# Performance work log

Hardware: AMD Instinct MI355X
Metric: run time of the kernel (lower is better)

The kernel has to match this reference:

```python
import jax, jax.numpy as jnp
import numpy as np

B, T, N, D = 16, 48, 256, 64
K_HEADS = 8


def setup_inputs() -> dict:
    key = jax.random.key(0)
    ks = jax.random.split(key, 12)
    return {
        "query": jax.random.normal(ks[0], (B, T, N, D), jnp.float32),
        "key": jax.random.normal(ks[1], (B, T, N, D), jnp.float32),
        "value": jax.random.normal(ks[2], (B, T, N, D), jnp.float32),
        "key_w": jax.random.normal(ks[3], (B, T, D, D), jnp.float32) * 0.05,
        "key_b": jax.random.normal(ks[4], (B, T, D), jnp.float32) * 0.05,
        "value_w": jax.random.normal(ks[5], (B, T, D, D), jnp.float32) * 0.05,
        "value_b": jax.random.normal(ks[6], (B, T, D), jnp.float32) * 0.05,
        "proj1_w": jax.random.normal(ks[7], (D, D), jnp.float32) * 0.05,
        "proj1_b": jax.random.normal(ks[8], (D,), jnp.float32) * 0.05,
        "proj2_w": jax.random.normal(ks[9], (D, D), jnp.float32) * 0.05,
        "proj2_b": jax.random.normal(ks[10], (D,), jnp.float32) * 0.05,
        "rate": jnp.full((1,), 0.8, jnp.float32),
    }


def reference(query, key, value, key_w, key_b, value_w, value_b,
              proj1_w, proj1_b, proj2_w, proj2_b, rate):
    b, t, n, d = query.shape
    hs = d // K_HEADS
    # per-(batch,time) projections (LinearCustom)
    k = jnp.einsum('btnd,btde->btne', key, key_w) + key_b[:, :, None, :]
    v = jnp.einsum('btnd,btde->btne', value, value_w) + value_b[:, :, None, :]
    # split heads along channel dim (matches torch.split on dim -1)
    qh = query.reshape(b, t, n, K_HEADS, hs)
    kh = k.reshape(b, t, n, K_HEADS, hs)
    vh = v.reshape(b, t, n, K_HEADS, hs)
    # scores: [b, h, n, q, k]
    scores = jnp.einsum('bqnhd,bknhd->bhnqk', qh, kh) / jnp.sqrt(jnp.asarray(hs, query.dtype))
    # time decay: b_time_decays[..., i, j] = (T-1-i) + 1 = T - i (depends on query pos only)
    dec = (t - jnp.arange(t, dtype=scores.dtype))[:, None]  # [T, 1], broadcasts over key axis
    s = jax.nn.sigmoid(scores)
    denom = 1.0 + jax.nn.sigmoid(s * jax.nn.sigmoid(rate) * dec)
    att = jax.nn.softmax(jnp.tanh(s / denom), axis=-1)
    x = jnp.einsum('bhnqk,bknhd->bqnhd', att, vh).reshape(b, t, n, d)
    x = jnp.tanh(x @ proj1_w.T + proj1_b)
    return x @ proj2_w.T + proj2_b
```

## Files before the change

kernel.cpp:

```cpp
#include <hip/hip_runtime.h>


#define B_ 16
#define T_ 48
#define N_ 256
#define D_ 64
#define H_ 8
#define HS_ 8

__device__ __forceinline__ float rcpf(float x) { return __builtin_amdgcn_rcpf(x); }

__global__ __launch_bounds__(256) void proj_kv_kernel(
    const float* __restrict__ key, const float* __restrict__ key_w, const float* __restrict__ key_b,
    const float* __restrict__ value, const float* __restrict__ value_w, const float* __restrict__ value_b,
    float* __restrict__ k_out, float* __restrict__ v_out)
{
    const int bt = blockIdx.x;
    const int which = blockIdx.y;
    const float* __restrict__ in = (which ? value : key) + (size_t)bt * N_ * D_;
    const float* __restrict__ w  = (which ? value_w : key_w) + (size_t)bt * D_ * D_;
    const float* __restrict__ bb = (which ? value_b : key_b) + (size_t)bt * D_;
    float* __restrict__ out = (which ? v_out : k_out) + (size_t)bt * N_ * D_;

    __shared__ float Wl[D_][D_];
    __shared__ float Xl[64][D_ + 1];
    __shared__ float Bl[D_];

    const int tid = threadIdx.x;
    #pragma unroll
    for (int i = tid; i < D_ * D_; i += 256) Wl[i >> 6][i & 63] = w[i];
    if (tid < D_) Bl[tid] = bb[tid];

    const int tc = tid & 15;
    const int tr = tid >> 4;

    for (int n0 = 0; n0 < N_; n0 += 64) {
        __syncthreads();
        #pragma unroll
        for (int i = tid; i < 64 * D_; i += 256) Xl[i >> 6][i & 63] = in[(size_t)n0 * D_ + i];
        __syncthreads();

        float acc[4][4];
        #pragma unroll
        for (int j = 0; j < 4; ++j) {
            #pragma unroll
            for (int i = 0; i < 4; ++i) acc[j][i] = Bl[tc * 4 + i];
        }

        #pragma unroll 8
        for (int d = 0; d < D_; ++d) {
            const float4 bv = *(const float4*)&Wl[d][tc * 4];
            #pragma unroll
            for (int j = 0; j < 4; ++j) {
                const float a = Xl[tr * 4 + j][d];
                acc[j][0] += a * bv.x;
                acc[j][1] += a * bv.y;
                acc[j][2] += a * bv.z;
                acc[j][3] += a * bv.w;
            }
        }

        #pragma unroll
        for (int j = 0; j < 4; ++j) {
            const float4 st = make_float4(acc[j][0], acc[j][1], acc[j][2], acc[j][3]);
            *(float4*)&out[(size_t)(n0 + tr * 4 + j) * D_ + tc * 4] = st;
        }
    }
}

__global__ __launch_bounds__(384) void attn_kernel(
    const float* __restrict__ query, float* __restrict__ k_xatt, const float* __restrict__ v_in,
    const float* __restrict__ rate)
{
    const int b = blockIdx.x >> 8;
    const int n = blockIdx.x & 255;

    __shared__ float Q[T_][68];
    __shared__ float K[T_][68];
    __shared__ float V[T_][68];

    const int tid = threadIdx.x;
    #pragma unroll
    for (int i = tid; i < T_ * D_; i += 384) {
        const int t = i >> 6, d = i & 63;
        const size_t g = ((size_t)(b * T_ + t) * N_ + n) * D_ + d;
        Q[t][d] = query[g];
        K[t][d] = k_xatt[g];
        V[t][d] = v_in[g];
    }
    const float rsig = rcpf(1.0f + __expf(-rate[0]));
    __syncthreads();

    const int q = tid % 48;
    const int h = tid / 48;
    float qf[8];
    #pragma unroll
    for (int d = 0; d < 8; ++d) qf[d] = Q[q][h * 8 + d];
    const float rd = rsig * (float)(T_ - q);

    float acc[8] = {0.f, 0.f, 0.f, 0.f, 0.f, 0.f, 0.f, 0.f};
    float ssum = 0.f;
    #pragma unroll 4
    for (int tk = 0; tk < T_; ++tk) {
        float sc = 0.f;
        #pragma unroll
        for (int d = 0; d < 8; ++d) sc += qf[d] * K[tk][h * 8 + d];
        sc *= 0.35355339059327373f;
        const float s   = rcpf(1.0f + __expf(-sc));
        const float s2  = rcpf(1.0f + __expf(-s * rd));
        const float arg = s * rcpf(1.0f + s2);
        const float th  = 1.0f - 2.0f * rcpf(__expf(2.0f * arg) + 1.0f);
        const float e   = __expf(th);
        ssum += e;
        #pragma unroll
        for (int d = 0; d < 8; ++d) acc[d] += e * V[tk][h * 8 + d];
    }
    const float inv = rcpf(ssum);

    __syncthreads();
    #pragma unroll
    for (int d = 0; d < 8; ++d) Q[q][h * 8 + d] = acc[d] * inv;
    __syncthreads();

    #pragma unroll
    for (int i = tid; i < T_ * D_; i += 384) {
        const int t = i >> 6, d = i & 63;
        k_xatt[((size_t)(b * T_ + t) * N_ + n) * D_ + d] = Q[t][d];
    }
}

__global__ __launch_bounds__(512) void out_proj_kernel(
    const float* __restrict__ xatt,
    const float* __restrict__ p1w, const float* __restrict__ p1b,
    const float* __restrict__ p2w, const float* __restrict__ p2b,
    float* __restrict__ out)
{
    __shared__ float W1t[D_][68];
    __shared__ float W2t[D_][68];
    __shared__ float X[64][68];
    __shared__ float B1[D_], B2[D_];

    const int tid = threadIdx.x;
    const size_t m0 = (size_t)blockIdx.x * 64;

    #pragma unroll
    for (int i = tid; i < D_ * D_; i += 512) {
        const int c = i >> 6, d = i & 63;
        W1t[d][c] = p1w[i];
        W2t[d][c] = p2w[i];
    }
    #pragma unroll
    for (int i = tid; i < 64 * D_; i += 512) X[i >> 6][i & 63] = xatt[m0 * D_ + i];
    if (tid < D_) { B1[tid] = p1b[tid]; B2[tid] = p2b[tid]; }
    __syncthreads();

    const int cg = tid & 7;
    const int r  = tid >> 3;

    float x1[8];
    {
        float a[8];
        #pragma unroll
        for (int i = 0; i < 8; ++i) a[i] = B1[cg * 8 + i];
        #pragma unroll 8
        for (int d = 0; d < D_; ++d) {
            const float xv = X[r][d];
            const float4 w0 = *(const float4*)&W1t[d][cg * 8];
            const float4 w1 = *(const float4*)&W1t[d][cg * 8 + 4];
            a[0] += xv * w0.x; a[1] += xv * w0.y; a[2] += xv * w0.z; a[3] += xv * w0.w;
            a[4] += xv * w1.x; a[5] += xv * w1.y; a[6] += xv * w1.z; a[7] += xv * w1.w;
        }
        #pragma unroll
        for (int i = 0; i < 8; ++i)
            x1[i] = 1.0f - 2.0f * rcpf(__expf(2.0f * a[i]) + 1.0f);
    }
    __syncthreads();
    #pragma unroll
    for (int i = 0; i < 8; ++i) X[r][cg * 8 + i] = x1[i];
    __syncthreads();

    {
        float a[8];
        #pragma unroll
        for (int i = 0; i < 8; ++i) a[i] = B2[cg * 8 + i];
        #pragma unroll 8
        for (int d = 0; d < D_; ++d) {
            const float xv = X[r][d];
            const float4 w0 = *(const float4*)&W2t[d][cg * 8];
            const float4 w1 = *(const float4*)&W2t[d][cg * 8 + 4];
            a[0] += xv * w0.x; a[1] += xv * w0.y; a[2] += xv * w0.z; a[3] += xv * w0.w;
            a[4] += xv * w1.x; a[5] += xv * w1.y; a[6] += xv * w1.z; a[7] += xv * w1.w;
        }
        const size_t og = (m0 + r) * D_ + cg * 8;
        *(float4*)&out[og]     = make_float4(a[0], a[1], a[2], a[3]);
        *(float4*)&out[og + 4] = make_float4(a[4], a[5], a[6], a[7]);
    }
}

extern "C" void kernel_launch(void* const* d_in, const int* in_sizes, int n_in,
                              void* d_out, int out_size, void* d_ws, size_t ws_size,
                              hipStream_t stream) {
    const float* query   = (const float*)d_in[0];
    const float* key     = (const float*)d_in[1];
    const float* value   = (const float*)d_in[2];
    const float* key_w   = (const float*)d_in[3];
    const float* key_b   = (const float*)d_in[4];
    const float* value_w = (const float*)d_in[5];
    const float* value_b = (const float*)d_in[6];
    const float* p1w     = (const float*)d_in[7];
    const float* p1b     = (const float*)d_in[8];
    const float* p2w     = (const float*)d_in[9];
    const float* p2b     = (const float*)d_in[10];
    const float* rate    = (const float*)d_in[11];
    float* out = (float*)d_out;

    float* kws = (float*)d_ws;
    float* vws = kws + (size_t)B_ * T_ * N_ * D_;

    dim3 gridA(B_ * T_, 2);
    proj_kv_kernel<<<gridA, 256, 0, stream>>>(key, key_w, key_b, value, value_w, value_b, kws, vws);
    attn_kernel<<<B_ * N_, 384, 0, stream>>>(query, kws, vws, rate);
    out_proj_kernel<<<(B_ * T_ * N_) / 64, 512, 0, stream>>>(kws, p1w, p1b, p2w, p2b, out);
}
```

Measured before the change: 259.3 us.

## Widen register tiles, vectorize loads, and use exp2 in all three kernels

Changes the K/V projection kernel to process 128 rows per pass with an 8-column-per-thread register tile. The out-projection kernel now handles 128 rows per block with two rows per thread, so weight loads from shared memory are reused more. Global and shared loads and stores become float4 in all kernels. The attention math is rewritten with exp2 and constants folded into the query scale. Larger per-thread tiles raise register pressure and halve the out-projection grid, which may lower occupancy.

```diff
diff --git a/kernel.cpp b/kernel.cpp
--- a/kernel.cpp
+++ b/kernel.cpp
@@ -9,6 +9,9 @@
 #define HS_ 8
 
 __device__ __forceinline__ float rcpf(float x) { return __builtin_amdgcn_rcpf(x); }
+__device__ __forceinline__ float ex2(float x) { return __builtin_amdgcn_exp2f(x); }
+
+#define LOG2E 1.4426950408889634f
 
 __global__ __launch_bounds__(256) void proj_kv_kernel(
     const float* __restrict__ key, const float* __restrict__ key_w, const float* __restrict__ key_b,
@@ -23,7 +26,7 @@
     float* __restrict__ out = (which ? v_out : k_out) + (size_t)bt * N_ * D_;
 
     __shared__ float Wl[D_][D_];
-    __shared__ float Xl[64][D_ + 1];
+    __shared__ float Xl[128][68];
     __shared__ float Bl[D_];
 
     const int tid = threadIdx.x;
@@ -31,39 +34,43 @@
     for (int i = tid; i < D_ * D_; i += 256) Wl[i >> 6][i & 63] = w[i];
     if (tid < D_) Bl[tid] = bb[tid];
 
-    const int tc = tid & 15;
-    const int tr = tid >> 4;
-
-    for (int n0 = 0; n0 < N_; n0 += 64) {
+    const int cg = tid & 7;
+    const int rg = tid >> 3;
+
+    for (int n0 = 0; n0 < N_; n0 += 128) {
         __syncthreads();
         #pragma unroll
-        for (int i = tid; i < 64 * D_; i += 256) Xl[i >> 6][i & 63] = in[(size_t)n0 * D_ + i];
+        for (int i = tid; i < 128 * D_ / 4; i += 256) {
+            const int e = i * 4;
+            *(float4*)&Xl[e >> 6][e & 63] = *(const float4*)&in[(size_t)n0 * D_ + e];
+        }
         __syncthreads();
 
-        float acc[4][4];
-        #pragma unroll
-        for (int j = 0; j < 4; ++j) {
+        float acc[4][8];
+        #pragma unroll
+        for (int j = 0; j < 4; ++j)
             #pragma unroll
-            for (int i = 0; i < 4; ++i) acc[j][i] = Bl[tc * 4 + i];
-        }
+            for (int i = 0; i < 8; ++i) acc[j][i] = Bl[cg * 8 + i];
 
         #pragma unroll 8
         for (int d = 0; d < D_; ++d) {
-            const float4 bv = *(const float4*)&Wl[d][tc * 4];
+            const float4 w0 = *(const float4*)&Wl[d][cg * 8];
+            const float4 w1 = *(const float4*)&Wl[d][cg * 8 + 4];
             #pragma unroll
             for (int j = 0; j < 4; ++j) {
-                const float a = Xl[tr * 4 + j][d];
-                acc[j][0] += a * bv.x;
-                acc[j][1] += a * bv.y;
-                acc[j][2] += a * bv.z;
-                acc[j][3] += a * bv.w;
+                const float a = Xl[rg + 32 * j][d];
+                acc[j][0] += a * w0.x; acc[j][1] += a * w0.y;
+                acc[j][2] += a * w0.z; acc[j][3] += a * w0.w;
+                acc[j][4] += a * w1.x; acc[j][5] += a * w1.y;
+                acc[j][6] += a * w1.z; acc[j][7] += a * w1.w;
             }
         }
 
         #pragma unroll
         for (int j = 0; j < 4; ++j) {
-            const float4 st = make_float4(acc[j][0], acc[j][1], acc[j][2], acc[j][3]);
-            *(float4*)&out[(size_t)(n0 + tr * 4 + j) * D_ + tc * 4] = st;
+            const size_t row = (size_t)(n0 + rg + 32 * j);
+            *(float4*)&out[row * D_ + cg * 8]     = make_float4(acc[j][0], acc[j][1], acc[j][2], acc[j][3]);
+            *(float4*)&out[row * D_ + cg * 8 + 4] = make_float4(acc[j][4], acc[j][5], acc[j][6], acc[j][7]);
         }
     }
 }
@@ -81,51 +88,61 @@
 
     const int tid = threadIdx.x;
     #pragma unroll
-    for (int i = tid; i < T_ * D_; i += 384) {
-        const int t = i >> 6, d = i & 63;
+    for (int i = tid; i < T_ * D_ / 4; i += 384) {
+        const int e = i * 4;
+        const int t = e >> 6, d = e & 63;
         const size_t g = ((size_t)(b * T_ + t) * N_ + n) * D_ + d;
-        Q[t][d] = query[g];
-        K[t][d] = k_xatt[g];
-        V[t][d] = v_in[g];
-    }
-    const float rsig = rcpf(1.0f + __expf(-rate[0]));
+        *(float4*)&Q[t][d] = *(const float4*)&query[g];
+        *(float4*)&K[t][d] = *(const float4*)&k_xatt[g];
+        *(float4*)&V[t][d] = *(const float4*)&v_in[g];
+    }
+    const float rsig = rcpf(1.0f + ex2(-rate[0] * LOG2E));
     __syncthreads();
 
     const int q = tid % 48;
     const int h = tid / 48;
-    float qf[8];
-    #pragma unroll
-    for (int d = 0; d < 8; ++d) qf[d] = Q[q][h * 8 + d];
-    const float rd = rsig * (float)(T_ - q);
-
-    float acc[8] = {0.f, 0.f, 0.f, 0.f, 0.f, 0.f, 0.f, 0.f};
+
+    const float C1 = 0.35355339059327373f * LOG2E;
+    float4 qa = *(const float4*)&Q[q][h * 8];
+    float4 qb = *(const float4*)&Q[q][h * 8 + 4];
+    qa.x *= -C1; qa.y *= -C1; qa.z *= -C1; qa.w *= -C1;
+    qb.x *= -C1; qb.y *= -C1; qb.z *= -C1; qb.w *= -C1;
+    const float rdn = -rsig * (float)(T_ - q) * LOG2E;
+
+    float4 acc0 = make_float4(0.f, 0.f, 0.f, 0.f);
+    float4 acc1 = make_float4(0.f, 0.f, 0.f, 0.f);
     float ssum = 0.f;
     #pragma unroll 4
     for (int tk = 0; tk < T_; ++tk) {
-        float sc = 0.f;
-        #pragma unroll
-        for (int d = 0; d < 8; ++d) sc += qf[d] * K[tk][h * 8 + d];
-        sc *= 0.35355339059327373f;
-        const float s   = rcpf(1.0f + __expf(-sc));
-        const float s2  = rcpf(1.0f + __expf(-s * rd));
+        const float4 ka = *(const float4*)&K[tk][h * 8];
+        const float4 kb = *(const float4*)&K[tk][h * 8 + 4];
+        const float dn = qa.x * ka.x + qa.y * ka.y + qa.z * ka.z + qa.w * ka.w
+                       + qb.x * kb.x + qb.y * kb.y + qb.z * kb.z + qb.w * kb.w;
+        const float s   = rcpf(1.0f + ex2(dn));
+        const float s2  = rcpf(1.0f + ex2(s * rdn));
         const float arg = s * rcpf(1.0f + s2);
-        const float th  = 1.0f - 2.0f * rcpf(__expf(2.0f * arg) + 1.0f);
-        const float e   = __expf(th);
+        const float th  = 1.0f - 2.0f * rcpf(ex2(arg * (2.0f * LOG2E)) + 1.0f);
+        const float e   = ex2(th * LOG2E);
         ssum += e;
-        #pragma unroll
-        for (int d = 0; d < 8; ++d) acc[d] += e * V[tk][h * 8 + d];
+        const float4 va = *(const float4*)&V[tk][h * 8];
+        const float4 vb = *(const float4*)&V[tk][h * 8 + 4];
+        acc0.x += e * va.x; acc0.y += e * va.y; acc0.z += e * va.z; acc0.w += e * va.w;
+        acc1.x += e * vb.x; acc1.y += e * vb.y; acc1.z += e * vb.z; acc1.w += e * vb.w;
     }
     const float inv = rcpf(ssum);
 
     __syncthreads();
-    #pragma unroll
-    for (int d = 0; d < 8; ++d) Q[q][h * 8 + d] = acc[d] * inv;
-    __syncthreads();
-
-    #pragma unroll
-    for (int i = tid; i < T_ * D_; i += 384) {
-        const int t = i >> 6, d = i & 63;
-        k_xatt[((size_t)(b * T_ + t) * N_ + n) * D_ + d] = Q[t][d];
+    acc0.x *= inv; acc0.y *= inv; acc0.z *= inv; acc0.w *= inv;
+    acc1.x *= inv; acc1.y *= inv; acc1.z *= inv; acc1.w *= inv;
+    *(float4*)&Q[q][h * 8]     = acc0;
+    *(float4*)&Q[q][h * 8 + 4] = acc1;
+    __syncthreads();
+
+    #pragma unroll
+    for (int i = tid; i < T_ * D_ / 4; i += 384) {
+        const int e = i * 4;
+        const int t = e >> 6, d = e & 63;
+        *(float4*)&k_xatt[((size_t)(b * T_ + t) * N_ + n) * D_ + d] = *(const float4*)&Q[t][d];
     }
 }
 
@@ -137,11 +154,11 @@
 {
     __shared__ float W1t[D_][68];
     __shared__ float W2t[D_][68];
-    __shared__ float X[64][68];
+    __shared__ float X[128][68];
     __shared__ float B1[D_], B2[D_];
 
     const int tid = threadIdx.x;
-    const size_t m0 = (size_t)blockIdx.x * 64;
+    const size_t m0 = (size_t)blockIdx.x * 128;
 
     #pragma unroll
     for (int i = tid; i < D_ * D_; i += 512) {
@@ -150,50 +167,67 @@
         W2t[d][c] = p2w[i];
     }
     #pragma unroll
-    for (int i = tid; i < 64 * D_; i += 512) X[i >> 6][i & 63] = xatt[m0 * D_ + i];
+    for (int i = tid; i < 128 * D_ / 4; i += 512) {
+        const int e = i * 4;
+        *(float4*)&X[e >> 6][e & 63] = *(const float4*)&xatt[m0 * D_ + e];
+    }
     if (tid < D_) { B1[tid] = p1b[tid]; B2[tid] = p2b[tid]; }
     __syncthreads();
 
     const int cg = tid & 7;
-    const int r  = tid >> 3;
-
-    float x1[8];
+    const int rp = tid >> 3;
+
+    float x1a[8], x1b[8];
     {
-        float a[8];
-        #pragma unroll
-        for (int i = 0; i < 8; ++i) a[i] = B1[cg * 8 + i];
+        float a[8], b2r[8];
+        #pragma unroll
+        for (int i = 0; i < 8; ++i) { a[i] = B1[cg * 8 + i]; b2r[i] = B1[cg * 8 + i]; }
         #pragma unroll 8
         for (int d = 0; d < D_; ++d) {
-            const float xv = X[r][d];
+            const float xv0 = X[rp][d];
+            const float xv1 = X[rp + 64][d];
             const float4 w0 = *(const float4*)&W1t[d][cg * 8];
             const float4 w1 = *(const float4*)&W1t[d][cg * 8 + 4];
-            a[0] += xv * w0.x; a[1] += xv * w0.y; a[2] += xv * w0.z; a[3] += xv * w0.w;
-            a[4] += xv * w1.x; a[5] += xv * w1.y; a[6] += xv * w1.z; a[7] += xv * w1.w;
-        }
-        #pragma unroll
-        for (int i = 0; i < 8; ++i)
-            x1[i] = 1.0f - 2.0f * rcpf(__expf(2.0f * a[i]) + 1.0f);
-    }
-    __syncthreads();
-    #pragma unroll
-    for (int i = 0; i < 8; ++i) X[r][cg * 8 + i] = x1[i];
+            a[0] += xv0 * w0.x; a[1] += xv0 * w0.y; a[2] += xv0 * w0.z; a[3] += xv0 * w0.w;
+            a[4] += xv0 * w1.x; a[5] += xv0 * w1.y; a[6] += xv0 * w1.z; a[7] += xv0 * w1.w;
+            b2r[0] += xv1 * w0.x; b2r[1] += xv1 * w0.y; b2r[2] += xv1 * w0.z; b2r[3] += xv1 * w0.w;
+            b2r[4] += xv1 * w1.x; b2r[5] += xv1 * w1.y; b2r[6] += xv1 * w1.z; b2r[7] += xv1 * w1.w;
+        }
+        #pragma unroll
+        for (int i = 0; i < 8; ++i) {
+            x1a[i] = 1.0f - 2.0f * rcpf(ex2(a[i]   * (2.0f * LOG2E)) + 1.0f);
+            x1b[i] = 1.0f - 2.0f * rcpf(ex2(b2r[i] * (2.0f * LOG2E)) + 1.0f);
+        }
+    }
+    __syncthreads();
+    #pragma unroll
+    for (int i = 0; i < 8; ++i) {
+        X[rp][cg * 8 + i]      = x1a[i];
+        X[rp + 64][cg * 8 + i] = x1b[i];
+    }
     __syncthreads();
 
     {
-        float a[8];
-        #pragma unroll
-        for (int i = 0; i < 8; ++i) a[i] = B2[cg * 8 + i];
+        float a[8], b2r[8];
+        #pragma unroll
+        for (int i = 0; i < 8; ++i) { a[i] = B2[cg * 8 + i]; b2r[i] = B2[cg * 8 + i]; }
         #pragma unroll 8
         for (int d = 0; d < D_; ++d) {
-            const float xv = X[r][d];
+            const float xv0 = X[rp][d];
+            const float xv1 = X[rp + 64][d];
             const float4 w0 = *(const float4*)&W2t[d][cg * 8];
             const float4 w1 = *(const float4*)&W2t[d][cg * 8 + 4];
-            a[0] += xv * w0.x; a[1] += xv * w0.y; a[2] += xv * w0.z; a[3] += xv * w0.w;
-            a[4] += xv * w1.x; a[5] += xv * w1.y; a[6] += xv * w1.z; a[7] += xv * w1.w;
-        }
-        const size_t og = (m0 + r) * D_ + cg * 8;
-        *(float4*)&out[og]     = make_float4(a[0], a[1], a[2], a[3]);
-        *(float4*)&out[og + 4] = make_float4(a[4], a[5], a[6], a[7]);
+            a[0] += xv0 * w0.x; a[1] += xv0 * w0.y; a[2] += xv0 * w0.z; a[3] += xv0 * w0.w;
+            a[4] += xv0 * w1.x; a[5] += xv0 * w1.y; a[6] += xv0 * w1.z; a[7] += xv0 * w1.w;
+            b2r[0] += xv1 * w0.x; b2r[1] += xv1 * w0.y; b2r[2] += xv1 * w0.z; b2r[3] += xv1 * w0.w;
+            b2r[4] += xv1 * w1.x; b2r[5] += xv1 * w1.y; b2r[6] += xv1 * w1.z; b2r[7] += xv1 * w1.w;
+        }
+        const size_t og0 = (m0 + rp) * D_ + cg * 8;
+        const size_t og1 = (m0 + rp + 64) * D_ + cg * 8;
+        *(float4*)&out[og0]     = make_float4(a[0], a[1], a[2], a[3]);
+        *(float4*)&out[og0 + 4] = make_float4(a[4], a[5], a[6], a[7]);
+        *(float4*)&out[og1]     = make_float4(b2r[0], b2r[1], b2r[2], b2r[3]);
+        *(float4*)&out[og1 + 4] = make_float4(b2r[4], b2r[5], b2r[6], b2r[7]);
     }
 }
 
@@ -220,5 +254,5 @@
     dim3 gridA(B_ * T_, 2);
     proj_kv_kernel<<<gridA, 256, 0, stream>>>(key, key_w, key_b, value, value_w, value_b, kws, vws);
     attn_kernel<<<B_ * N_, 384, 0, stream>>>(query, kws, vws, rate);
-    out_proj_kernel<<<(B_ * T_ * N_) / 64, 512, 0, stream>>>(kws, p1w, p1b, p2w, p2b, out);
-}
+    out_proj_kernel<<<(B_ * T_ * N_) / 128, 512, 0, stream>>>(kws, p1w, p1b, p2w, p2b, out);
+}
```

After: 222.8 us. -14.1%, faster.
